# Performance work log

Hardware: AMD Instinct MI355X
Metric: run time of the kernel (lower is better)

## Reference

```python
import jax, jax.numpy as jnp
import numpy as np

# Arbitrary non-contiguous kernel tap offsets (constructor arg sk_ind)
SK_IND = np.array([-512, -256, -128, -96, -64, -48, -32, -24, -16, -12, -8, -6,
                   -4, -3, -2, -1, 0, 1, 2, 3, 4, 6, 8, 12, 16, 24, 32, 48,
                   64, 96, 128, 256], dtype=np.int32)
IN_CHANNELS = 64
OUT_CHANNELS = 64
BATCH = 16
INPUT_LEN = 4096


def setup_inputs() -> dict:
    key = jax.random.key(0)
    k1, k2 = jax.random.split(key)
    x = jax.random.normal(k1, (BATCH, IN_CHANNELS, INPUT_LEN), dtype=jnp.float32)
    sk_weights = jax.random.normal(k2, (OUT_CHANNELS, IN_CHANNELS, SK_IND.shape[0]), dtype=jnp.float32)
    return {"x": x, "sk_weights": sk_weights}


def reference(x, sk_weights):
    # x: [B, Cin, L]; sk_weights: [Cout, Cin, K]
    B, C, L = x.shape
    low_pad = max(-int(SK_IND.min()), 0)   # zeros consumed by negative taps
    high_pad = max(int(SK_IND.max()), 0)   # zeros consumed by positive taps
    # Original pads zeros AFTER the signal: [x, zeros(high_pad), zeros(low_pad)];
    # negative numpy indices then wrap into the trailing low_pad zeros.
    padded = jnp.concatenate([x, jnp.zeros((B, C, high_pad + low_pad), x.dtype)], axis=-1)
    padded_len = L + high_pad + low_pad
    idx = SK_IND[:, None] + np.arange(L)                 # [K, L], static
    idx = np.where(idx < 0, padded_len + idx, idx)       # emulate numpy negative-index wrap
    gathered = padded[:, :, idx]                          # [B, Cin, K, L]
    # Per-position GEMM: contract over (Cin, K)
    return jnp.einsum('oik,bikl->bol', sk_weights, gathered)  # [B, Cout, L]
```

## Files before the change

kernel.cpp:

```cpp
#include <hip/hip_runtime.h>


#define B_    16
#define CIN   64
#define COUT  64
#define LEN   4096
#define PAD_LO 512
#define PAD_HI 256
#define LPAD  (LEN + PAD_LO + PAD_HI)
#define NTAP  32

typedef float f32x4 __attribute__((ext_vector_type(4)));
typedef short bf16x8_s __attribute__((ext_vector_type(8)));
typedef __bf16 bf16x8_b __attribute__((ext_vector_type(8)));
typedef unsigned short u16x8 __attribute__((ext_vector_type(8)));

template <typename V>
static __device__ inline auto mfma_16x16x32_bf16(V a, V b, f32x4 c, int)
    -> decltype(__builtin_amdgcn_mfma_f32_16x16x32_bf16(a, b, c, 0, 0, 0)) {
  return __builtin_amdgcn_mfma_f32_16x16x32_bf16(a, b, c, 0, 0, 0);
}
template <typename V>
static __device__ inline f32x4 mfma_16x16x32_bf16(V a, V b, f32x4 c, long) {
  return __builtin_amdgcn_mfma_f32_16x16x32_bf16(
      __builtin_bit_cast(bf16x8_b, a), __builtin_bit_cast(bf16x8_b, b), c, 0, 0, 0);
}

static __device__ inline unsigned short f32_to_bf16_rne(float f) {
  unsigned int u = __builtin_bit_cast(unsigned int, f);
  u += 0x7fffu + ((u >> 16) & 1u);
  return (unsigned short)(u >> 16);
}

static __device__ inline void async_copy16(const void* g, void* l) {
  __builtin_amdgcn_global_load_lds((const __attribute__((address_space(1))) unsigned int*)g,
                                   (__attribute__((address_space(3))) unsigned int*)l, 16, 0, 0);
}

__global__ __launch_bounds__(256) void prep_x(const float* __restrict__ x,
                                              unsigned short* __restrict__ xp) {
  __shared__ float tile[64][65];
  const int b = blockIdx.y;
  const int lp0 = blockIdx.x * 64;
  const int tid = threadIdx.x;
  const bool data = (lp0 >= PAD_LO) && (lp0 < PAD_LO + LEN);
  if (data) {
    const int l0 = lp0 - PAD_LO;
#pragma unroll
    for (int it = 0; it < 4; ++it) {
      const int pidx = it * 256 + tid;
      const int il = pidx >> 4;
      const int lq = (pidx & 15) * 4;
      const float4 v = *(const float4*)&x[(size_t)(b * CIN + il) * LEN + l0 + lq];
      tile[lq + 0][il] = v.x;
      tile[lq + 1][il] = v.y;
      tile[lq + 2][il] = v.z;
      tile[lq + 3][il] = v.w;
    }
  }
  __syncthreads();
#pragma unroll
  for (int it = 0; it < 2; ++it) {
    const int pidx = it * 256 + tid;
    const int ll = pidx >> 3;
    const int i8 = (pidx & 7) * 8;
    u16x8 v = {0, 0, 0, 0, 0, 0, 0, 0};
    if (data) {
#pragma unroll
      for (int j = 0; j < 8; ++j) v[j] = f32_to_bf16_rne(tile[ll][i8 + j]);
    }
    *(u16x8*)&xp[(size_t)(b * LPAD + lp0 + ll) * CIN + i8] = v;
  }
}

__global__ __launch_bounds__(256) void prep_w(const float* __restrict__ w,
                                              unsigned short* __restrict__ wf) {
  const int e = blockIdx.x * 256 + threadIdx.x;
  const int j = e & 7;
  const int lane = (e >> 3) & 63;
  const int m = (e >> 9) & 3;
  const int c = (e >> 11) & 1;
  const int t = e >> 12;
  const int q = lane >> 4, r = lane & 15;
  const int o = m * 16 + r;
  const int i = c * 32 + q * 8 + j;
  wf[e] = f32_to_bf16_rne(w[(size_t)(o * CIN + i) * NTAP + t]);
}

__global__ __launch_bounds__(256, 2) void sconv_main(const unsigned short* __restrict__ xp,
                                                     const unsigned short* __restrict__ wf,
                                                     float* __restrict__ out) {
  constexpr int TAP[NTAP] = {-512, -256, -128, -96, -64, -48, -32, -24, -16, -12, -8,
                             -6,   -4,   -3,   -2,  -1,  0,   1,   2,   3,   4,  6,
                             8,    12,   16,   24,  32,  48,  64,  96,  128, 256};
  __shared__ alignas(16) char smem[81920];

  const int id = blockIdx.x;
  const int b = id >> 4;
  const int l0 = (id & 15) * 256;
  const int lb = l0 + PAD_LO;
  const int tid = threadIdx.x;
  const int wv = tid >> 6, lane = tid & 63;
  const int q = lane >> 4, r = lane & 15;

  const char* xbase = (const char*)xp + ((size_t)b * LPAD + lb) * (CIN * 2);
  const char* wbase = (const char*)wf;

  auto stageW = [&](int t) {
    const char* src = wbase + t * 8192;
    char* dst = smem + (t & 1) * 8192;
#pragma unroll
    for (int it = 0; it < 2; ++it)
      async_copy16(src + (it * 256 + wv * 64 + lane) * 16,
                   dst + (it * 256 + wv * 64) * 16);
  };
  auto stageB = [&](int a0, int ng) {
    for (int g = wv; g < ng; g += 4) {
      const int ra = a0 + g * 8 + (lane >> 3);
      const int ch = (lane & 7) ^ (ra & 7);
      const int sb = (lb + a0 + g * 8) & 511;
      async_copy16(xbase + (ptrdiff_t)ra * 128 + ch * 16, smem + 16384 + sb * 128);
    }
  };

  f32x4 acc[4][4] = {};

  stageW(0);
  stageB(-512, 32);

#pragma unroll
  for (int t = 0; t < NTAP; ++t) {
    __syncthreads();
    if (t + 1 < NTAP) {
      stageW(t + 1);
      const int dstart = TAP[t] + 256;
      const int dend = TAP[t + 1] + 256;
      const int a0 = dstart & ~7;
      stageB(a0, (dend - a0 + 7) >> 3);
    }
    __builtin_amdgcn_sched_barrier(0);

    const int e = (TAP[t] + r) & 7;
    int baddr[4];
#pragma unroll
    for (int n = 0; n < 4; ++n) {
      const int slot = (lb + TAP[t] + wv * 64 + 16 * n + r) & 511;
      baddr[n] = 16384 + slot * 128 + ((q ^ e) << 4);
    }
#pragma unroll
    for (int c = 0; c < 2; ++c) {
      bf16x8_s A[4], Bf[4];
#pragma unroll
      for (int m = 0; m < 4; ++m)
        A[m] = *(const bf16x8_s*)(smem + (t & 1) * 8192 + (c * 4 + m) * 1024 + lane * 16);
#pragma unroll
      for (int n = 0; n < 4; ++n)
        Bf[n] = *(const bf16x8_s*)(smem + (baddr[n] ^ (c << 6)));
#pragma unroll
      for (int m = 0; m < 4; ++m)
#pragma unroll
        for (int n = 0; n < 4; ++n)
          acc[m][n] = mfma_16x16x32_bf16(A[m], Bf[n], acc[m][n], 0);
    }
  }

#pragma unroll
  for (int m = 0; m < 4; ++m)
#pragma unroll
    for (int n = 0; n < 4; ++n)
#pragma unroll
      for (int d = 0; d < 4; ++d) {
        const int o = 16 * m + 4 * q + d;
        const int l = l0 + wv * 64 + 16 * n + r;
        out[((size_t)b * COUT + o) * LEN + l] = acc[m][n][d];
      }
}

extern "C" void kernel_launch(void* const* d_in, const int* in_sizes, int n_in,
                              void* d_out, int out_size, void* d_ws, size_t ws_size,
                              hipStream_t stream) {
  const float* x = (const float*)d_in[0];
  const float* w = (const float*)d_in[1];
  float* out = (float*)d_out;

  unsigned short* xp = (unsigned short*)d_ws;
  unsigned short* wfp = xp + (size_t)B_ * LPAD * CIN;

  prep_x<<<dim3(LPAD / 64, B_), 256, 0, stream>>>(x, xp);
  prep_w<<<dim3((NTAP * 2 * 4 * 64 * 8) / 256), 256, 0, stream>>>(w, wfp);
  sconv_main<<<dim3(B_ * 16), 256, 0, stream>>>(xp, wfp, out);
}
```

Baseline: 93.97 us.

## Split main conv over input-channel halves with LDS reduction and smaller tiles

Halves the per-block sequence tile from 256 to 128 positions, doubling the grid to 512 blocks so more of the GPU's compute units are occupied. Within a block, waves are split two ways by position and two ways by input-channel half, and the halves' accumulators are combined through LDS before the store. The block index mapping also interleaves batches. The cost is extra halo loading relative to useful work, a final LDS reduction with two more barriers, and writes done by only half the waves.

```diff
diff --git a/kernel.cpp b/kernel.cpp
--- a/kernel.cpp
+++ b/kernel.cpp
@@ -96,19 +96,20 @@
   __shared__ alignas(16) char smem[81920];
 
   const int id = blockIdx.x;
-  const int b = id >> 4;
-  const int l0 = (id & 15) * 256;
+  const int b = (id & 7) * 2 + ((id >> 3) & 1);
+  const int l0 = (id >> 4) * 128;
   const int lb = l0 + PAD_LO;
   const int tid = threadIdx.x;
   const int wv = tid >> 6, lane = tid & 63;
   const int q = lane >> 4, r = lane & 15;
+  const int lh = wv & 1, ch = wv >> 1;
 
   const char* xbase = (const char*)xp + ((size_t)b * LPAD + lb) * (CIN * 2);
   const char* wbase = (const char*)wf;
 
   auto stageW = [&](int t) {
     const char* src = wbase + t * 8192;
-    char* dst = smem + (t & 1) * 8192;
+    char* dst = smem + 65536 + (t & 1) * 8192;
 #pragma unroll
     for (int it = 0; it < 2; ++it)
       async_copy16(src + (it * 256 + wv * 64 + lane) * 16,
@@ -117,63 +118,71 @@
   auto stageB = [&](int a0, int ng) {
     for (int g = wv; g < ng; g += 4) {
       const int ra = a0 + g * 8 + (lane >> 3);
-      const int ch = (lane & 7) ^ (ra & 7);
+      const int cs = (lane & 7) ^ (ra & 7);
       const int sb = (lb + a0 + g * 8) & 511;
-      async_copy16(xbase + (ptrdiff_t)ra * 128 + ch * 16, smem + 16384 + sb * 128);
+      async_copy16(xbase + (ptrdiff_t)ra * 128 + cs * 16, smem + sb * 128);
     }
   };
 
   f32x4 acc[4][4] = {};
 
   stageW(0);
-  stageB(-512, 32);
+  stageB(-512, 16);
 
 #pragma unroll
   for (int t = 0; t < NTAP; ++t) {
     __syncthreads();
     if (t + 1 < NTAP) {
       stageW(t + 1);
-      const int dstart = TAP[t] + 256;
-      const int dend = TAP[t + 1] + 256;
+      const int dstart = TAP[t] + 128;
+      const int dend = TAP[t + 1] + 128;
       const int a0 = dstart & ~7;
       stageB(a0, (dend - a0 + 7) >> 3);
     }
     __builtin_amdgcn_sched_barrier(0);
 
     const int e = (TAP[t] + r) & 7;
-    int baddr[4];
+    const char* Wb = smem + 65536 + (t & 1) * 8192 + ch * 4096;
+    bf16x8_s A[4], Bf[4];
+#pragma unroll
+    for (int m = 0; m < 4; ++m)
+      A[m] = *(const bf16x8_s*)(Wb + m * 1024 + lane * 16);
 #pragma unroll
     for (int n = 0; n < 4; ++n) {
-      const int slot = (lb + TAP[t] + wv * 64 + 16 * n + r) & 511;
-      baddr[n] = 16384 + slot * 128 + ((q ^ e) << 4);
-    }
-#pragma unroll
-    for (int c = 0; c < 2; ++c) {
-      bf16x8_s A[4], Bf[4];
-#pragma unroll
-      for (int m = 0; m < 4; ++m)
-        A[m] = *(const bf16x8_s*)(smem + (t & 1) * 8192 + (c * 4 + m) * 1024 + lane * 16);
+      const int slot = (lb + TAP[t] + lh * 64 + 16 * n + r) & 511;
+      Bf[n] = *(const bf16x8_s*)(smem + slot * 128 + (((ch * 4 + q) ^ e) << 4));
+    }
+#pragma unroll
+    for (int m = 0; m < 4; ++m)
 #pragma unroll
       for (int n = 0; n < 4; ++n)
-        Bf[n] = *(const bf16x8_s*)(smem + (baddr[n] ^ (c << 6)));
-#pragma unroll
-      for (int m = 0; m < 4; ++m)
-#pragma unroll
-        for (int n = 0; n < 4; ++n)
-          acc[m][n] = mfma_16x16x32_bf16(A[m], Bf[n], acc[m][n], 0);
-    }
-  }
-
-#pragma unroll
-  for (int m = 0; m < 4; ++m)
-#pragma unroll
-    for (int n = 0; n < 4; ++n)
-#pragma unroll
-      for (int d = 0; d < 4; ++d) {
-        const int o = 16 * m + 4 * q + d;
-        const int l = l0 + wv * 64 + 16 * n + r;
-        out[((size_t)b * COUT + o) * LEN + l] = acc[m][n][d];
+        acc[m][n] = mfma_16x16x32_bf16(A[m], Bf[n], acc[m][n], 0);
+  }
+
+  __syncthreads();
+  if (ch == 1) {
+#pragma unroll
+    for (int m = 0; m < 4; ++m)
+#pragma unroll
+      for (int n = 0; n < 4; ++n)
+        *(f32x4*)(smem + lh * 16384 + ((m * 4 + n) * 64 + lane) * 16) = acc[m][n];
+  }
+  __syncthreads();
+  if (ch == 0) {
+#pragma unroll
+    for (int m = 0; m < 4; ++m)
+#pragma unroll
+      for (int n = 0; n < 4; ++n) {
+        const f32x4 other = *(const f32x4*)(smem + lh * 16384 + ((m * 4 + n) * 64 + lane) * 16);
+        const f32x4 v = acc[m][n] + other;
+#pragma unroll
+        for (int d = 0; d < 4; ++d) {
+          const int o = 16 * m + 4 * q + d;
+          const int l = l0 + lh * 64 + 16 * n + r;
+          out[((size_t)b * COUT + o) * LEN + l] = v[d];
+        }
       }
+  }
 }
 
 extern "C" void kernel_launch(void* const* d_in, const int* in_sizes, int n_in,
@@ -188,5 +197,5 @@
 
   prep_x<<<dim3(LPAD / 64, B_), 256, 0, stream>>>(x, xp);
   prep_w<<<dim3((NTAP * 2 * 4 * 64 * 8) / 256), 256, 0, stream>>>(w, wfp);
-  sconv_main<<<dim3(B_ * 16), 256, 0, stream>>>(xp, wfp, out);
-}
+  sconv_main<<<dim3(16 * 32), 256, 0, stream>>>(xp, wfp, out);
+}
```

Result: no change. 92.50 us (-1.6%).
